# Kernel tuning notes

Hardware: AMD Instinct MI355X
Metric: run time of the kernel (lower is better)

## Reference

```python
import jax, jax.numpy as jnp
import numpy as np

B, S, E, H = 1, 2048, 1024, 16
D = E // H          # head_dim = 64
SM_SCALE = 0.5      # module default, not 1/sqrt(D)


def setup_inputs() -> dict:
    key = jax.random.key(0)
    ks = jax.random.split(key, 9)
    std = 0.02
    return {
        "x":  jax.random.normal(ks[0], (B, S, E), dtype=jnp.float32),
        "Wq": jax.random.normal(ks[1], (E, E), dtype=jnp.float32) * std,
        "bq": jnp.zeros((E,), dtype=jnp.float32),
        "Wk": jax.random.normal(ks[2], (E, E), dtype=jnp.float32) * std,
        "bk": jnp.zeros((E,), dtype=jnp.float32),
        "Wv": jax.random.normal(ks[3], (E, E), dtype=jnp.float32) * std,
        "bv": jnp.zeros((E,), dtype=jnp.float32),
        "Wo": jax.random.normal(ks[4], (E, E), dtype=jnp.float32) * std,
        "bo": jnp.zeros((E,), dtype=jnp.float32),
    }


def _split_heads(t):
    # [B,S,E] -> [B,H,S,D]
    b, s, _ = t.shape
    return jnp.transpose(t.reshape(b, s, H, D), (0, 2, 1, 3))


def reference(x, Wq, bq, Wk, bk, Wv, bv, Wo, bo):
    # Projections in fp32, then cast to bf16 (matches module's .astype(bf16))
    q = _split_heads((x @ Wq + bq).astype(jnp.bfloat16))
    k = _split_heads((x @ Wk + bk).astype(jnp.bfloat16))
    v = _split_heads((x @ Wv + bv).astype(jnp.bfloat16))

    # Blockwise loop in the original is mathematically full causal attention
    scores = jnp.einsum("bhqd,bhkd->bhqk", q, k) * SM_SCALE  # [B,H,S,S] bf16
    causal = jnp.tril(jnp.ones((S, S), dtype=bool))
    scores = jnp.where(causal[None, None, :, :], scores, -jnp.inf)
    probs = jax.nn.softmax(scores, axis=-1)
    out = jnp.einsum("bhqk,bhkd->bhqd", probs, v)            # [B,H,S,D]

    out = jnp.transpose(out, (0, 2, 1, 3)).reshape(B, S, E)
    # dropout off (is_training=False / rate=0); final projection in fp32
    return out.astype(jnp.float32) @ Wo + bo
```

## Files before the change

kernel.cpp:

```cpp
#include <hip/hip_runtime.h>
#include <hip/hip_bf16.h>

#define S_LEN 2048
#define E_DIM 1024
#define NH    16
#define HD    64
#define SM_SCALE 0.5f

typedef short bf16x8_t  __attribute__((ext_vector_type(8)));
typedef float f32x4_t   __attribute__((ext_vector_type(4)));
typedef float f32x16_t  __attribute__((ext_vector_type(16)));
typedef __bf16 bf16x4_t __attribute__((ext_vector_type(4)));

static __device__ __forceinline__ unsigned short f2bf_bits(float f) {
    return __builtin_bit_cast(unsigned short, (__bf16)f);
}

#define GLD16(gp, lp) __builtin_amdgcn_global_load_lds(                       \
    (const __attribute__((address_space(1))) void*)(gp),                      \
    (__attribute__((address_space(3))) void*)(lp), 16, 0, 0)

__global__ void k_prep(const float* __restrict__ x,
                       const float* __restrict__ Wq, const float* __restrict__ Wk,
                       const float* __restrict__ Wv, const float* __restrict__ Wo,
                       __bf16* __restrict__ xb, __bf16* __restrict__ wt) {
    const int z = blockIdx.z;
    if (z < 4) {
        __shared__ float tile[32][33];
        const float* W = z == 0 ? Wq : z == 1 ? Wk : z == 2 ? Wv : Wo;
        __bf16* o = wt + (size_t)z * E_DIM * E_DIM;
        const int tx = threadIdx.x, ty = threadIdx.y;
        const int bx = blockIdx.x * 32, by = blockIdx.y * 32;
#pragma unroll
        for (int j = 0; j < 32; j += 8)
            tile[ty + j][tx] = W[(size_t)(by + ty + j) * E_DIM + bx + tx];
        __syncthreads();
#pragma unroll
        for (int j = 0; j < 32; j += 8)
            o[(size_t)(bx + ty + j) * E_DIM + by + tx] = (__bf16)tile[tx][ty + j];
    } else {
        const int bid = (z - 4) * 1024 + blockIdx.y * 32 + blockIdx.x;
        const int tid = threadIdx.y * 32 + threadIdx.x;
        const int i = bid * 256 + tid;
        const float4 v = ((const float4*)x)[i];
        bf16x4_t o4;
        o4.x = (__bf16)v.x; o4.y = (__bf16)v.y; o4.z = (__bf16)v.z; o4.w = (__bf16)v.w;
        ((bf16x4_t*)xb)[i] = o4;
    }
}

__global__ __launch_bounds__(256) void k_gemm_qkv(
    const __bf16* __restrict__ xb, const __bf16* __restrict__ wt,
    const float* __restrict__ bq, const float* __restrict__ bk, const float* __restrict__ bv,
    __bf16* __restrict__ qkv) {
    __shared__ __align__(16) unsigned short As[128 * 32];
    __shared__ __align__(16) unsigned short Bs[128 * 32];

    const int z = blockIdx.z;
    const __bf16* Bt = wt + (size_t)z * E_DIM * E_DIM;
    const float* bias = z == 0 ? bq : z == 1 ? bk : bv;
    __bf16* out = qkv + (size_t)z * NH * S_LEN * HD;

    const int tid = threadIdx.x, w = tid >> 6, l = tid & 63;
    const int lm = l & 15, q4 = l >> 4;
    const int bm = blockIdx.y, bn = blockIdx.x;
    const int wm = w >> 1, wn = w & 1;

    const int sm = (w << 4) + (l >> 2);
    const int skk = (l & 3) << 3;
    const __bf16* Ag = xb + (size_t)(bm * 128 + sm) * E_DIM + skk;
    const __bf16* Bg = Bt + (size_t)(bn * 128 + sm) * E_DIM + skk;
    unsigned short* AsW = As + (w << 9);
    unsigned short* BsW = Bs + (w << 9);

    f32x4_t acc[4][4];
#pragma unroll
    for (int i = 0; i < 4; i++)
#pragma unroll
        for (int j = 0; j < 4; j++) { acc[i][j].x = 0.f; acc[i][j].y = 0.f; acc[i][j].z = 0.f; acc[i][j].w = 0.f; }

    for (int k0 = 0; k0 < E_DIM; k0 += 32) {
        __syncthreads();
        GLD16(Ag + k0, AsW);
        GLD16(Ag + (size_t)64 * E_DIM + k0, AsW + 2048);
        GLD16(Bg + k0, BsW);
        GLD16(Bg + (size_t)64 * E_DIM + k0, BsW + 2048);
        __syncthreads();

        bf16x8_t af[4], bfr[4];
#pragma unroll
        for (int mt = 0; mt < 4; mt++)
            af[mt] = *(const bf16x8_t*)&As[(wm * 64 + mt * 16 + lm) * 32 + q4 * 8];
#pragma unroll
        for (int nt = 0; nt < 4; nt++)
            bfr[nt] = *(const bf16x8_t*)&Bs[(wn * 64 + nt * 16 + lm) * 32 + q4 * 8];
#pragma unroll
        for (int mt = 0; mt < 4; mt++)
#pragma unroll
            for (int nt = 0; nt < 4; nt++)
                acc[mt][nt] = __builtin_amdgcn_mfma_f32_16x16x32_bf16(af[mt], bfr[nt], acc[mt][nt], 0, 0, 0);
    }

#pragma unroll
    for (int nt = 0; nt < 4; nt++) {
        const int n = bn * 128 + wn * 64 + nt * 16 + lm;
        const float bval = bias[n];
        const int h = n >> 6, d = n & 63;
        const int tile0 = bm * 2 + wm;
        if (z == 2) {
            const int db = d >> 5, dl = d & 31;
#pragma unroll
            for (int mt = 0; mt < 4; mt++) {
                __bf16* ob = out + (((size_t)h * 32 + tile0) * 8 + db * 4 + mt) * 512
                                 + (dl + (q4 >> 1) * 32) * 8 + (q4 & 1) * 4;
                union { unsigned short s4[4]; uint2 u; } pk;
#pragma unroll
                for (int i = 0; i < 4; i++) pk.s4[i] = f2bf_bits(acc[mt][nt][i] + bval);
                *(uint2*)ob = pk.u;
            }
        } else {
            const float scale = (z == 0) ? SM_SCALE : 1.0f;
            const int kc = d >> 4, khalf = (d >> 3) & 1, j = d & 7;
#pragma unroll
            for (int mt = 0; mt < 4; mt++) {
                __bf16* ob = out + (((size_t)h * 32 + tile0) * 8 + (mt >> 1) * 4 + kc) * 512
                                 + ((mt & 1) * 16 + q4 * 4 + khalf * 32) * 8 + j;
#pragma unroll
                for (int i = 0; i < 4; i++)
                    ob[i * 8] = (__bf16)((acc[mt][nt][i] + bval) * scale);
            }
        }
    }
}

__global__ __launch_bounds__(256, 2) void k_attn(
    const __bf16* __restrict__ Qf, const __bf16* __restrict__ Kf, const __bf16* __restrict__ Vf,
    __bf16* __restrict__ attn) {
    __shared__ __align__(16) unsigned short KVs[2][2][4096];
    __shared__ __align__(16) unsigned short Pl[4][32 * 40];

    const int b = blockIdx.x;
    int qt, h;
    if (b < 256) { qt = 16 + (b >> 4); h = b & 15; }
    else         { qt = 15 - ((b - 256) >> 4); h = (b - 256) & 15; }

    const int tid = threadIdx.x, w = tid >> 6, l = tid & 63;
    const int rh = w & 1, kh = w >> 1;
    const int l31 = l & 31, lh = l >> 5;

    const __bf16* Qb = Qf + ((size_t)h * 32 + qt) * 4096;
    const __bf16* Kb = Kf + (size_t)h * 32 * 4096;
    const __bf16* Vb = Vf + (size_t)h * 32 * 4096;

    bf16x8_t qf[4];
#pragma unroll
    for (int kc = 0; kc < 4; kc++)
        qf[kc] = *(const bf16x8_t*)(Qb + ((rh * 4 + kc) << 9) + l * 8);

    float lacc = 0.f;
    f32x16_t oacc[2];
#pragma unroll
    for (int db = 0; db < 2; db++)
#pragma unroll
        for (int r = 0; r < 16; r++) oacc[db][r] = 0.f;

    unsigned short* Pw = Pl[w];

    GLD16(Kb + (w << 9) + l * 8,       &KVs[0][0][(w << 9) + l * 8]);
    GLD16(Kb + ((w + 4) << 9) + l * 8, &KVs[0][0][((w + 4) << 9) + l * 8]);
    GLD16(Vb + (w << 9) + l * 8,       &KVs[0][1][(w << 9) + l * 8]);
    GLD16(Vb + ((w + 4) << 9) + l * 8, &KVs[0][1][((w + 4) << 9) + l * 8]);
    __syncthreads();

    for (int s = 0; s <= qt; s++) {
        const int bb = s & 1;
        if (s < qt) {
            const __bf16* Kg = Kb + (size_t)(s + 1) * 4096;
            const __bf16* Vg = Vb + (size_t)(s + 1) * 4096;
            GLD16(Kg + (w << 9) + l * 8,       &KVs[bb ^ 1][0][(w << 9) + l * 8]);
            GLD16(Kg + ((w + 4) << 9) + l * 8, &KVs[bb ^ 1][0][((w + 4) << 9) + l * 8]);
            GLD16(Vg + (w << 9) + l * 8,       &KVs[bb ^ 1][1][(w << 9) + l * 8]);
            GLD16(Vg + ((w + 4) << 9) + l * 8, &KVs[bb ^ 1][1][((w + 4) << 9) + l * 8]);
        }

        const bool diag = (s == qt);
        if (!(diag && kh > rh)) {
            f32x16_t st;
#pragma unroll
            for (int r = 0; r < 16; r++) st[r] = 0.f;
#pragma unroll
            for (int kc = 0; kc < 4; kc++) {
                bf16x8_t kf = *(const bf16x8_t*)&KVs[bb][0][((kh * 4 + kc) << 9) + l * 8];
                st = __builtin_amdgcn_mfma_f32_32x32x16_bf16(kf, qf[kc], st, 0, 0, 0);
            }
            if (diag && kh == rh) {
#pragma unroll
                for (int r = 0; r < 16; r++) {
                    const int keyl = (r & 3) + 8 * (r >> 2) + 4 * lh;
                    st[r] = (keyl > l31) ? 0.f : __expf(st[r]);
                }
            } else {
#pragma unroll
                for (int r = 0; r < 16; r++) st[r] = __expf(st[r]);
            }
#pragma unroll
            for (int r = 0; r < 16; r++) lacc += st[r];
#pragma unroll
            for (int a = 0; a < 4; a++) {
                union { unsigned short s4[4]; uint2 u; } pk;
#pragma unroll
                for (int i = 0; i < 4; i++) pk.s4[i] = f2bf_bits(st[a * 4 + i]);
                *(uint2*)&Pw[l31 * 40 + lh * 4 + a * 8] = pk.u;
            }
#pragma unroll
            for (int c = 0; c < 2; c++) {
                bf16x8_t pf = *(const bf16x8_t*)&Pw[l31 * 40 + c * 16 + lh * 8];
#pragma unroll
                for (int db = 0; db < 2; db++) {
                    bf16x8_t vf = *(const bf16x8_t*)&KVs[bb][1][((db * 4 + kh * 2 + c) << 9) + l * 8];
                    oacc[db] = __builtin_amdgcn_mfma_f32_32x32x16_bf16(vf, pf, oacc[db], 0, 0, 0);
                }
            }
        }
        __syncthreads();
    }

    __syncthreads();
    float* Ex = (float*)KVs;
    if (kh == 1) {
        float* e = Ex + (rh * 64 + l) * 34;
#pragma unroll
        for (int db = 0; db < 2; db++)
#pragma unroll
            for (int r = 0; r < 16; r++) e[db * 16 + r] = oacc[db][r];
        e[32] = lacc;
    }
    __syncthreads();
    if (kh == 0) {
        const float* e = Ex + (rh * 64 + l) * 34;
#pragma unroll
        for (int db = 0; db < 2; db++)
#pragma unroll
            for (int r = 0; r < 16; r++) oacc[db][r] += e[db * 16 + r];
        lacc += e[32];
        lacc += __shfl_xor(lacc, 32, 64);
        const float rl = 1.f / lacc;
        const int row = qt * 64 + rh * 32 + l31;
#pragma unroll
        for (int db = 0; db < 2; db++)
#pragma unroll
            for (int a = 0; a < 4; a++) {
                union { unsigned short s4[4]; uint2 u; } pk;
#pragma unroll
                for (int i = 0; i < 4; i++) pk.s4[i] = f2bf_bits(oacc[db][a * 4 + i] * rl);
                *(uint2*)(attn + (size_t)row * E_DIM + h * HD + db * 32 + a * 8 + lh * 4) = pk.u;
            }
    }
}

__global__ __launch_bounds__(256) void k_gemm_out(
    const __bf16* __restrict__ A, const __bf16* __restrict__ Bt,
    const float* __restrict__ bias, float* __restrict__ out) {
    __shared__ __align__(16) unsigned short As[2][64 * 32];
    __shared__ __align__(16) unsigned short Bs[2][128 * 32];

    const int tid = threadIdx.x, w = tid >> 6, l = tid & 63;
    const int lm = l & 15, q4 = l >> 4;
    const int bm = blockIdx.y, bn = blockIdx.x;
    const int wm = w >> 1, wn = w & 1;

    const int sm = (w << 4) + (l >> 2);
    const int skk = (l & 3) << 3;
    const __bf16* Ag = A + (size_t)(bm * 64 + sm) * E_DIM + skk;
    const __bf16* Bg = Bt + (size_t)(bn * 128 + sm) * E_DIM + skk;
    const int woff = w << 9;

    f32x4_t acc[2][4];
#pragma unroll
    for (int i = 0; i < 2; i++)
#pragma unroll
        for (int j = 0; j < 4; j++) { acc[i][j].x = 0.f; acc[i][j].y = 0.f; acc[i][j].z = 0.f; acc[i][j].w = 0.f; }

    GLD16(Ag, &As[0][woff]);
    GLD16(Bg, &Bs[0][woff]);
    GLD16(Bg + (size_t)64 * E_DIM, &Bs[0][woff + 2048]);
    __syncthreads();

    for (int s = 0; s < 32; s++) {
        const int bb = s & 1;
        if (s < 31) {
            const int k0 = (s + 1) * 32;
            GLD16(Ag + k0, &As[bb ^ 1][woff]);
            GLD16(Bg + k0, &Bs[bb ^ 1][woff]);
            GLD16(Bg + (size_t)64 * E_DIM + k0, &Bs[bb ^ 1][woff + 2048]);
        }

        bf16x8_t af[2], bfr[4];
#pragma unroll
        for (int mt = 0; mt < 2; mt++)
            af[mt] = *(const bf16x8_t*)&As[bb][(wm * 32 + mt * 16 + lm) * 32 + q4 * 8];
#pragma unroll
        for (int nt = 0; nt < 4; nt++)
            bfr[nt] = *(const bf16x8_t*)&Bs[bb][(wn * 64 + nt * 16 + lm) * 32 + q4 * 8];
#pragma unroll
        for (int mt = 0; mt < 2; mt++)
#pragma unroll
            for (int nt = 0; nt < 4; nt++)
                acc[mt][nt] = __builtin_amdgcn_mfma_f32_16x16x32_bf16(af[mt], bfr[nt], acc[mt][nt], 0, 0, 0);
        __syncthreads();
    }

#pragma unroll
    for (int nt = 0; nt < 4; nt++) {
        const int n = bn * 128 + wn * 64 + nt * 16 + lm;
        const float bval = bias[n];
#pragma unroll
        for (int mt = 0; mt < 2; mt++) {
            const int r0 = bm * 64 + wm * 32 + mt * 16 + q4 * 4;
#pragma unroll
            for (int i = 0; i < 4; i++)
                out[(size_t)(r0 + i) * E_DIM + n] = acc[mt][nt][i] + bval;
        }
    }
}

extern "C" void kernel_launch(void* const* d_in, const int* in_sizes, int n_in,
                              void* d_out, int out_size, void* d_ws, size_t ws_size,
                              hipStream_t stream) {
    const float* x  = (const float*)d_in[0];
    const float* Wq = (const float*)d_in[1];
    const float* bq = (const float*)d_in[2];
    const float* Wk = (const float*)d_in[3];
    const float* bk = (const float*)d_in[4];
    const float* Wv = (const float*)d_in[5];
    const float* bv = (const float*)d_in[6];
    const float* Wo = (const float*)d_in[7];
    const float* bo = (const float*)d_in[8];
    float* out = (float*)d_out;

    char* ws = (char*)d_ws;
    __bf16* xb   = (__bf16*)(ws);
    __bf16* wt   = (__bf16*)(ws + ((size_t)4  << 20));
    __bf16* qkv  = (__bf16*)(ws + ((size_t)12 << 20));
    __bf16* attn = (__bf16*)(ws + ((size_t)24 << 20));

    k_prep<<<dim3(32, 32, 6), dim3(32, 8), 0, stream>>>(x, Wq, Wk, Wv, Wo, xb, wt);
    k_gemm_qkv<<<dim3(E_DIM / 128, S_LEN / 128, 3), 256, 0, stream>>>(xb, wt, bq, bk, bv, qkv);
    k_attn<<<dim3(512), 256, 0, stream>>>(
        qkv, qkv + (size_t)NH * S_LEN * HD, qkv + (size_t)2 * NH * S_LEN * HD, attn);
    k_gemm_out<<<dim3(E_DIM / 128, S_LEN / 64), 256, 0, stream>>>(
        attn, wt + (size_t)3 * E_DIM * E_DIM, bo, out);
}
```

Baseline: 154.4 us.

## Double-buffer QKV GEMM loads and pair causal q-tiles per attention block

After: 158.1 us. 1.02x slower.

```diff
diff --git a/kernel.cpp b/kernel.cpp
--- a/kernel.cpp
+++ b/kernel.cpp
@@ -53,8 +53,8 @@
     const __bf16* __restrict__ xb, const __bf16* __restrict__ wt,
     const float* __restrict__ bq, const float* __restrict__ bk, const float* __restrict__ bv,
     __bf16* __restrict__ qkv) {
-    __shared__ __align__(16) unsigned short As[128 * 32];
-    __shared__ __align__(16) unsigned short Bs[128 * 32];
+    __shared__ __align__(16) unsigned short As[2][128 * 32];
+    __shared__ __align__(16) unsigned short Bs[2][128 * 32];
 
     const int z = blockIdx.z;
     const __bf16* Bt = wt + (size_t)z * E_DIM * E_DIM;
@@ -70,8 +70,7 @@
     const int skk = (l & 3) << 3;
     const __bf16* Ag = xb + (size_t)(bm * 128 + sm) * E_DIM + skk;
     const __bf16* Bg = Bt + (size_t)(bn * 128 + sm) * E_DIM + skk;
-    unsigned short* AsW = As + (w << 9);
-    unsigned short* BsW = Bs + (w << 9);
+    const int woff = w << 9;
 
     f32x4_t acc[4][4];
 #pragma unroll
@@ -79,26 +78,35 @@
 #pragma unroll
         for (int j = 0; j < 4; j++) { acc[i][j].x = 0.f; acc[i][j].y = 0.f; acc[i][j].z = 0.f; acc[i][j].w = 0.f; }
 
-    for (int k0 = 0; k0 < E_DIM; k0 += 32) {
-        __syncthreads();
-        GLD16(Ag + k0, AsW);
-        GLD16(Ag + (size_t)64 * E_DIM + k0, AsW + 2048);
-        GLD16(Bg + k0, BsW);
-        GLD16(Bg + (size_t)64 * E_DIM + k0, BsW + 2048);
-        __syncthreads();
+    GLD16(Ag, &As[0][woff]);
+    GLD16(Ag + (size_t)64 * E_DIM, &As[0][woff + 2048]);
+    GLD16(Bg, &Bs[0][woff]);
+    GLD16(Bg + (size_t)64 * E_DIM, &Bs[0][woff + 2048]);
+    __syncthreads();
+
+    for (int s = 0; s < 32; s++) {
+        const int bb = s & 1;
+        if (s < 31) {
+            const int k0 = (s + 1) * 32;
+            GLD16(Ag + k0, &As[bb ^ 1][woff]);
+            GLD16(Ag + (size_t)64 * E_DIM + k0, &As[bb ^ 1][woff + 2048]);
+            GLD16(Bg + k0, &Bs[bb ^ 1][woff]);
+            GLD16(Bg + (size_t)64 * E_DIM + k0, &Bs[bb ^ 1][woff + 2048]);
+        }
 
         bf16x8_t af[4], bfr[4];
 #pragma unroll
         for (int mt = 0; mt < 4; mt++)
-            af[mt] = *(const bf16x8_t*)&As[(wm * 64 + mt * 16 + lm) * 32 + q4 * 8];
+            af[mt] = *(const bf16x8_t*)&As[bb][(wm * 64 + mt * 16 + lm) * 32 + q4 * 8];
 #pragma unroll
         for (int nt = 0; nt < 4; nt++)
-            bfr[nt] = *(const bf16x8_t*)&Bs[(wn * 64 + nt * 16 + lm) * 32 + q4 * 8];
+            bfr[nt] = *(const bf16x8_t*)&Bs[bb][(wn * 64 + nt * 16 + lm) * 32 + q4 * 8];
 #pragma unroll
         for (int mt = 0; mt < 4; mt++)
 #pragma unroll
             for (int nt = 0; nt < 4; nt++)
                 acc[mt][nt] = __builtin_amdgcn_mfma_f32_16x16x32_bf16(af[mt], bfr[nt], acc[mt][nt], 0, 0, 0);
+        __syncthreads();
     }
 
 #pragma unroll
@@ -140,121 +148,124 @@
     __shared__ __align__(16) unsigned short Pl[4][32 * 40];
 
     const int b = blockIdx.x;
-    int qt, h;
-    if (b < 256) { qt = 16 + (b >> 4); h = b & 15; }
-    else         { qt = 15 - ((b - 256) >> 4); h = (b - 256) & 15; }
+    const int pi = b >> 4, h = b & 15;
 
     const int tid = threadIdx.x, w = tid >> 6, l = tid & 63;
     const int rh = w & 1, kh = w >> 1;
     const int l31 = l & 31, lh = l >> 5;
 
-    const __bf16* Qb = Qf + ((size_t)h * 32 + qt) * 4096;
     const __bf16* Kb = Kf + (size_t)h * 32 * 4096;
     const __bf16* Vb = Vf + (size_t)h * 32 * 4096;
 
-    bf16x8_t qf[4];
-#pragma unroll
-    for (int kc = 0; kc < 4; kc++)
-        qf[kc] = *(const bf16x8_t*)(Qb + ((rh * 4 + kc) << 9) + l * 8);
-
-    float lacc = 0.f;
-    f32x16_t oacc[2];
-#pragma unroll
-    for (int db = 0; db < 2; db++)
-#pragma unroll
-        for (int r = 0; r < 16; r++) oacc[db][r] = 0.f;
-
     unsigned short* Pw = Pl[w];
 
-    GLD16(Kb + (w << 9) + l * 8,       &KVs[0][0][(w << 9) + l * 8]);
-    GLD16(Kb + ((w + 4) << 9) + l * 8, &KVs[0][0][((w + 4) << 9) + l * 8]);
-    GLD16(Vb + (w << 9) + l * 8,       &KVs[0][1][(w << 9) + l * 8]);
-    GLD16(Vb + ((w + 4) << 9) + l * 8, &KVs[0][1][((w + 4) << 9) + l * 8]);
-    __syncthreads();
-
-    for (int s = 0; s <= qt; s++) {
-        const int bb = s & 1;
-        if (s < qt) {
-            const __bf16* Kg = Kb + (size_t)(s + 1) * 4096;
-            const __bf16* Vg = Vb + (size_t)(s + 1) * 4096;
-            GLD16(Kg + (w << 9) + l * 8,       &KVs[bb ^ 1][0][(w << 9) + l * 8]);
-            GLD16(Kg + ((w + 4) << 9) + l * 8, &KVs[bb ^ 1][0][((w + 4) << 9) + l * 8]);
-            GLD16(Vg + (w << 9) + l * 8,       &KVs[bb ^ 1][1][(w << 9) + l * 8]);
-            GLD16(Vg + ((w + 4) << 9) + l * 8, &KVs[bb ^ 1][1][((w + 4) << 9) + l * 8]);
-        }
-
-        const bool diag = (s == qt);
-        if (!(diag && kh > rh)) {
-            f32x16_t st;
-#pragma unroll
-            for (int r = 0; r < 16; r++) st[r] = 0.f;
-#pragma unroll
-            for (int kc = 0; kc < 4; kc++) {
-                bf16x8_t kf = *(const bf16x8_t*)&KVs[bb][0][((kh * 4 + kc) << 9) + l * 8];
-                st = __builtin_amdgcn_mfma_f32_32x32x16_bf16(kf, qf[kc], st, 0, 0, 0);
+#pragma unroll
+    for (int job = 0; job < 2; job++) {
+        const int qt = job ? (31 - pi) : pi;
+        const __bf16* Qb = Qf + ((size_t)h * 32 + qt) * 4096;
+
+        bf16x8_t qf[4];
+#pragma unroll
+        for (int kc = 0; kc < 4; kc++)
+            qf[kc] = *(const bf16x8_t*)(Qb + ((rh * 4 + kc) << 9) + l * 8);
+
+        float lacc = 0.f;
+        f32x16_t oacc[2];
+#pragma unroll
+        for (int db = 0; db < 2; db++)
+#pragma unroll
+            for (int r = 0; r < 16; r++) oacc[db][r] = 0.f;
+
+        GLD16(Kb + (w << 9) + l * 8,       &KVs[0][0][(w << 9) + l * 8]);
+        GLD16(Kb + ((w + 4) << 9) + l * 8, &KVs[0][0][((w + 4) << 9) + l * 8]);
+        GLD16(Vb + (w << 9) + l * 8,       &KVs[0][1][(w << 9) + l * 8]);
+        GLD16(Vb + ((w + 4) << 9) + l * 8, &KVs[0][1][((w + 4) << 9) + l * 8]);
+        __syncthreads();
+
+        for (int s = 0; s <= qt; s++) {
+            const int bb = s & 1;
+            if (s < qt) {
+                const __bf16* Kg = Kb + (size_t)(s + 1) * 4096;
+                const __bf16* Vg = Vb + (size_t)(s + 1) * 4096;
+                GLD16(Kg + (w << 9) + l * 8,       &KVs[bb ^ 1][0][(w << 9) + l * 8]);
+                GLD16(Kg + ((w + 4) << 9) + l * 8, &KVs[bb ^ 1][0][((w + 4) << 9) + l * 8]);
+                GLD16(Vg + (w << 9) + l * 8,       &KVs[bb ^ 1][1][(w << 9) + l * 8]);
+                GLD16(Vg + ((w + 4) << 9) + l * 8, &KVs[bb ^ 1][1][((w + 4) << 9) + l * 8]);
             }
-            if (diag && kh == rh) {
-#pragma unroll
-                for (int r = 0; r < 16; r++) {
-                    const int keyl = (r & 3) + 8 * (r >> 2) + 4 * lh;
-                    st[r] = (keyl > l31) ? 0.f : __expf(st[r]);
-                }
-            } else {
-#pragma unroll
-                for (int r = 0; r < 16; r++) st[r] = __expf(st[r]);
+
+            const bool diag = (s == qt);
+            if (!(diag && kh > rh)) {
+                f32x16_t st;
+#pragma unroll
+                for (int r = 0; r < 16; r++) st[r] = 0.f;
+#pragma unroll
+                for (int kc = 0; kc < 4; kc++) {
+                    bf16x8_t kf = *(const bf16x8_t*)&KVs[bb][0][((kh * 4 + kc) << 9) + l * 8];
+                    st = __builtin_amdgcn_mfma_f32_32x32x16_bf16(kf, qf[kc], st, 0, 0, 0);
+                }
+                if (diag && kh == rh) {
+#pragma unroll
+                    for (int r = 0; r < 16; r++) {
+                        const int keyl = (r & 3) + 8 * (r >> 2) + 4 * lh;
+                        st[r] = (keyl > l31) ? 0.f : __expf(st[r]);
+                    }
+                } else {
+#pragma unroll
+                    for (int r = 0; r < 16; r++) st[r] = __expf(st[r]);
+                }
+#pragma unroll
+                for (int r = 0; r < 16; r++) lacc += st[r];
+#pragma unroll
+                for (int a = 0; a < 4; a++) {
+                    union { unsigned short s4[4]; uint2 u; } pk;
+#pragma unroll
+                    for (int i = 0; i < 4; i++) pk.s4[i] = f2bf_bits(st[a * 4 + i]);
+                    *(uint2*)&Pw[l31 * 40 + lh * 4 + a * 8] = pk.u;
+                }
+#pragma unroll
+                for (int c = 0; c < 2; c++) {
+                    bf16x8_t pf = *(const bf16x8_t*)&Pw[l31 * 40 + c * 16 + lh * 8];
+#pragma unroll
+                    for (int db = 0; db < 2; db++) {
+                        bf16x8_t vf = *(const bf16x8_t*)&KVs[bb][1][((db * 4 + kh * 2 + c) << 9) + l * 8];
+                        oacc[db] = __builtin_amdgcn_mfma_f32_32x32x16_bf16(vf, pf, oacc[db], 0, 0, 0);
+                    }
+                }
             }
-#pragma unroll
-            for (int r = 0; r < 16; r++) lacc += st[r];
-#pragma unroll
-            for (int a = 0; a < 4; a++) {
-                union { unsigned short s4[4]; uint2 u; } pk;
-#pragma unroll
-                for (int i = 0; i < 4; i++) pk.s4[i] = f2bf_bits(st[a * 4 + i]);
-                *(uint2*)&Pw[l31 * 40 + lh * 4 + a * 8] = pk.u;
-            }
-#pragma unroll
-            for (int c = 0; c < 2; c++) {
-                bf16x8_t pf = *(const bf16x8_t*)&Pw[l31 * 40 + c * 16 + lh * 8];
-#pragma unroll
-                for (int db = 0; db < 2; db++) {
-                    bf16x8_t vf = *(const bf16x8_t*)&KVs[bb][1][((db * 4 + kh * 2 + c) << 9) + l * 8];
-                    oacc[db] = __builtin_amdgcn_mfma_f32_32x32x16_bf16(vf, pf, oacc[db], 0, 0, 0);
-                }
-            }
-        }
-        __syncthreads();
-    }
-
-    __syncthreads();
-    float* Ex = (float*)KVs;
-    if (kh == 1) {
-        float* e = Ex + (rh * 64 + l) * 34;
-#pragma unroll
-        for (int db = 0; db < 2; db++)
-#pragma unroll
-            for (int r = 0; r < 16; r++) e[db * 16 + r] = oacc[db][r];
-        e[32] = lacc;
-    }
-    __syncthreads();
-    if (kh == 0) {
-        const float* e = Ex + (rh * 64 + l) * 34;
-#pragma unroll
-        for (int db = 0; db < 2; db++)
-#pragma unroll
-            for (int r = 0; r < 16; r++) oacc[db][r] += e[db * 16 + r];
-        lacc += e[32];
-        lacc += __shfl_xor(lacc, 32, 64);
-        const float rl = 1.f / lacc;
-        const int row = qt * 64 + rh * 32 + l31;
-#pragma unroll
-        for (int db = 0; db < 2; db++)
-#pragma unroll
-            for (int a = 0; a < 4; a++) {
-                union { unsigned short s4[4]; uint2 u; } pk;
-#pragma unroll
-                for (int i = 0; i < 4; i++) pk.s4[i] = f2bf_bits(oacc[db][a * 4 + i] * rl);
-                *(uint2*)(attn + (size_t)row * E_DIM + h * HD + db * 32 + a * 8 + lh * 4) = pk.u;
-            }
+            __syncthreads();
+        }
+
+        float* Ex = (float*)KVs;
+        if (kh == 1) {
+            float* e = Ex + (rh * 64 + l) * 34;
+#pragma unroll
+            for (int db = 0; db < 2; db++)
+#pragma unroll
+                for (int r = 0; r < 16; r++) e[db * 16 + r] = oacc[db][r];
+            e[32] = lacc;
+        }
+        __syncthreads();
+        if (kh == 0) {
+            const float* e = Ex + (rh * 64 + l) * 34;
+#pragma unroll
+            for (int db = 0; db < 2; db++)
+#pragma unroll
+                for (int r = 0; r < 16; r++) oacc[db][r] += e[db * 16 + r];
+            lacc += e[32];
+            lacc += __shfl_xor(lacc, 32, 64);
+            const float rl = 1.f / lacc;
+            const int row = qt * 64 + rh * 32 + l31;
+#pragma unroll
+            for (int db = 0; db < 2; db++)
+#pragma unroll
+                for (int a = 0; a < 4; a++) {
+                    union { unsigned short s4[4]; uint2 u; } pk;
+#pragma unroll
+                    for (int i = 0; i < 4; i++) pk.s4[i] = f2bf_bits(oacc[db][a * 4 + i] * rl);
+                    *(uint2*)(attn + (size_t)row * E_DIM + h * HD + db * 32 + a * 8 + lh * 4) = pk.u;
+                }
+        }
+        __syncthreads();
     }
 }
 
@@ -346,7 +357,7 @@
 
     k_prep<<<dim3(32, 32, 6), dim3(32, 8), 0, stream>>>(x, Wq, Wk, Wv, Wo, xb, wt);
     k_gemm_qkv<<<dim3(E_DIM / 128, S_LEN / 128, 3), 256, 0, stream>>>(xb, wt, bq, bk, bv, qkv);
-    k_attn<<<dim3(512), 256, 0, stream>>>(
+    k_attn<<<dim3(256), 256, 0, stream>>>(
         qkv, qkv + (size_t)NH * S_LEN * HD, qkv + (size_t)2 * NH * S_LEN * HD, attn);
     k_gemm_out<<<dim3(E_DIM / 128, S_LEN / 64), 256, 0, stream>>>(
         attn, wt + (size_t)3 * E_DIM * E_DIM, bo, out);
```
